# Kernel tuning notes

Measured on AMD Instinct MI355X. Metric: run time of the kernel, lower is better.

## Reference

```python
import jax, jax.numpy as jnp
import numpy as np


def _rx(state, theta, axis):
    # Apply RX(theta) to qubit at tensor axis `axis`. state: (B, 2,...,2) complex.
    half = theta * 0.5
    c = jnp.cos(half)
    s = jnp.sin(half)
    a0 = jnp.take(state, 0, axis=axis)
    a1 = jnp.take(state, 1, axis=axis)
    return jnp.stack([c * a0 - 1j * s * a1, c * a1 - 1j * s * a0], axis=axis)


def _cnot(state, w):
    # CNOT with control wire w (axis w+1), target wire w+1 (axis w+2).
    c_ax = w + 1
    s0 = jnp.take(state, 0, axis=c_ax)
    # after removing the control axis, the target axis index becomes c_ax
    s1 = jnp.flip(jnp.take(state, 1, axis=c_ax), axis=c_ax)
    return jnp.stack([s0, s1], axis=c_ax)


def _run_circuit(x, params):
    # x: (B, n) encoding angles; params: (depth, n) trainable RX angles.
    B, n = x.shape
    depth = params.shape[0]
    state = jnp.zeros((B,) + (2,) * n, jnp.complex64)
    state = state.at[(slice(None),) + (0,) * n].set(1.0 + 0.0j)
    # angle encoding: RX(x_w) on each wire
    for w in range(n):
        theta = x[:, w].reshape((B,) + (1,) * (n - 1))
        state = _rx(state, theta, w + 1)
    # variational layers: RX(param) per wire, then CNOT chain
    for d in range(depth):
        for w in range(n):
            state = _rx(state, params[d, w], w + 1)
        for w in range(n - 1):
            state = _cnot(state, w)
    probs = state.real ** 2 + state.imag ** 2  # (B, 2,...,2)
    ez = []
    for w in range(n):
        axes = tuple(a for a in range(1, n + 1) if a != w + 1)
        p = probs.sum(axes)  # (B, 2)
        ez.append(p[:, 0] - p[:, 1])  # <Z_w>
    return jnp.stack(ez, axis=1)  # (B, n)


def setup_inputs() -> dict:
    key = jax.random.key(0)
    k0, k1, k2, k3, k4 = jax.random.split(key, 5)
    seq_len, batch, input_dim = 256, 128, 64
    n_qubits, depth, hidden = 10, 2, 256
    inputs = jax.random.normal(k0, (seq_len, batch, input_dim), jnp.float32)
    mask = jax.random.randint(k1, (seq_len, batch), 0, 2).astype(jnp.int32)
    qparams = jax.random.normal(k2, (4, depth, n_qubits), jnp.float32)
    W = jax.random.normal(k3, (4, hidden, n_qubits), jnp.float32) / np.sqrt(n_qubits)
    b = jax.random.normal(k4, (4, hidden), jnp.float32) * 0.01
    return {"inputs": inputs, "mask": mask, "qparams": qparams, "W": W, "b": b}


def reference(inputs, mask, qparams, W, b):
    seq_len, batch, _ = inputs.shape
    n = qparams.shape[-1]
    hidden = W.shape[1]
    maskf = mask.astype(inputs.dtype)

    circuits4 = jax.vmap(_run_circuit, in_axes=(None, 0))  # over the 4 gates

    def step(carry, xm):
        hx, cx = carry
        x_t, m_t = xm
        q_in = jnp.concatenate([x_t, hx], axis=1)[:, :n]  # (B, n)
        z = circuits4(q_in, qparams)                      # (4, B, n)
        pre = jnp.einsum('gbn,ghn->gbh', z, W) + b[:, None, :]
        f = jax.nn.sigmoid(pre[0])
        i = jax.nn.sigmoid(pre[1])
        g = jnp.tanh(pre[2])
        o = jax.nn.sigmoid(pre[3])
        m = m_t[:, None]
        f = f * m + (1.0 - m)
        i = i * m
        g = g * m
        o = o * m + (1.0 - m)
        cx_new = f * cx + i * g
        hx_new = o * jnp.tanh(cx_new)
        return (hx_new, cx_new), hx_new

    h0 = jnp.zeros((batch, hidden), inputs.dtype)
    c0 = jnp.zeros((batch, hidden), inputs.dtype)
    (hx, cx), outputs = jax.lax.scan(jax.checkpoint(step), (h0, c0), (inputs, maskf))
    return outputs, (hx, cx)
```

## Files before the change

kernel.cpp:

```cpp
#include <hip/hip_runtime.h>

#define T_LEN 256
#define BATCH 128
#define NQ 10
#define HID 256
#define OUT_HX (T_LEN * BATCH * HID)
#define OUT_CX (OUT_HX + BATCH * HID)
#define TROW 33

#define KS  (-1.44269504089f)
#define KT2 (-2.88539008178f)

__global__ __launch_bounds__(256) void zker(
    const float* __restrict__ inputs,
    const float* __restrict__ qparams,
    float* __restrict__ zws)
{
  const int b   = blockIdx.x;
  const int tq  = blockIdx.y;
  const int tid = threadIdx.x;
  const int t   = tq * 64 + (tid >> 2);
  const int g   = tid & 3;

  const float sg = (g == 2) ? KT2 : KS;

  float th0[NQ], cth[NQ], sth[NQ];
#pragma unroll
  for (int k = 0; k < NQ; ++k) {
    th0[k]   = qparams[g * 2 * NQ + k];
    float t1 = qparams[g * 2 * NQ + NQ + k];
    sth[k] = __sinf(t1);
    cth[k] = __cosf(t1);
  }
  float cphi[NQ], sphi[NQ];
  const float* xp = inputs + (t * BATCH + b) * 64;
#pragma unroll
  for (int k = 0; k < NQ; ++k) {
    float ang = xp[k] + th0[k];
    sphi[k] = __sinf(ang);
    cphi[k] = __cosf(ang);
  }
  float* zout = zws + (b * NQ * T_LEN + t) * 4 + g;
#pragma unroll
  for (int w = 0; w < NQ; ++w) {
    float vI, vZ, vY, vX; int js;
    if (w == NQ - 1) { vI = 0.f; vZ = cth[NQ-1]; vY = sth[NQ-1]; vX = 0.f; js = NQ - 2; }
    else             { vI = 1.f; vZ = 0.f; vY = 0.f; vX = 0.f; js = w; }
#pragma unroll
    for (int j = js; j >= 0; --j) {
      float nI = cth[j] * (cphi[j+1] * vZ - sphi[j+1] * vY);
      float nZ = cth[j] * vI;
      float nY = sth[j] * vX;
      float nX = -sth[j] * (sphi[j+1] * vZ + cphi[j+1] * vY);
      vI = nI; vZ = nZ; vY = nY; vX = nX;
    }
    zout[w * T_LEN * 4] = (vI + cphi[0] * vZ - sphi[0] * vY) * sg;
  }
}

__global__ __launch_bounds__(512) void scanker(
    const float* __restrict__ zws,
    const int*  __restrict__ mask,
    const float* __restrict__ W,
    const float* __restrict__ bias,
    float* __restrict__ out)
{
  const int b    = blockIdx.x;
  const int h0   = blockIdx.y * 32;
  const int tid  = threadIdx.x;
  const int lane = tid & 63;
  const int wavu = __builtin_amdgcn_readfirstlane(tid >> 6);

  __shared__ float tlds[2][64 * TROW];
  __shared__ float mk[T_LEN];

  for (int t = tid; t < T_LEN; t += 512) mk[t] = (float)mask[t * BATCH + b];
  __syncthreads();

  int srcA[6]; bool pm[6];
#pragma unroll
  for (int k = 0; k < 6; ++k) {
    const int d = 1 << k;
    pm[k]   = (lane >= d);
    srcA[k] = ((lane >= d) ? (lane - d) : lane) << 2;
  }

  float bsc[4][4];
#pragma unroll
  for (int hh = 0; hh < 4; ++hh) {
    const int h = __builtin_amdgcn_readfirstlane(h0 + wavu * 4 + hh);
    bsc[hh][0] = bias[0 * HID + h] * KS;
    bsc[hh][1] = bias[1 * HID + h] * KS;
    bsc[hh][2] = bias[2 * HID + h] * KT2;
    bsc[hh][3] = bias[3 * HID + h] * KS;
  }

  float carry[4];
#pragma unroll
  for (int i = 0; i < 4; ++i) carry[i] = 0.f;

  const float4* zg = (const float4*)zws + b * NQ * T_LEN;

  for (int r = 0; r < 4; ++r) {
    const int p = r & 1;
    const int t = r * 64 + lane;
    const float m = mk[t];
    const float onem = 1.f - m;

    float acc[4][4];
#pragma unroll
    for (int hh = 0; hh < 4; ++hh) {
      acc[hh][0] = bsc[hh][0]; acc[hh][1] = bsc[hh][1];
      acc[hh][2] = bsc[hh][2]; acc[hh][3] = bsc[hh][3];
    }
#pragma unroll
    for (int n = 0; n < NQ; ++n) {
      const float4 z = zg[n * T_LEN + t];
#pragma unroll
      for (int hh = 0; hh < 4; ++hh) {
        const int wb = __builtin_amdgcn_readfirstlane((h0 + wavu * 4 + hh) * NQ + n);
        acc[hh][0] = fmaf(z.x, W[0 * HID * NQ + wb], acc[hh][0]);
        acc[hh][1] = fmaf(z.y, W[1 * HID * NQ + wb], acc[hh][1]);
        acc[hh][2] = fmaf(z.z, W[2 * HID * NQ + wb], acc[hh][2]);
        acc[hh][3] = fmaf(z.w, W[3 * HID * NQ + wb], acc[hh][3]);
      }
    }

    float a4[4], w4[4], om4[4];
#pragma unroll
    for (int hh = 0; hh < 4; ++hh) {
      const float uf = __builtin_amdgcn_rcpf(1.f + __builtin_amdgcn_exp2f(acc[hh][0]));
      const float ui = __builtin_amdgcn_rcpf(1.f + __builtin_amdgcn_exp2f(acc[hh][1]));
      const float ug = __builtin_amdgcn_rcpf(1.f + __builtin_amdgcn_exp2f(acc[hh][2]));
      const float uo = __builtin_amdgcn_rcpf(1.f + __builtin_amdgcn_exp2f(acc[hh][3]));
      a4[hh]  = fmaf(m, uf, onem);
      w4[hh]  = m * ui * fmaf(2.f, ug, -1.f);
      om4[hh] = fmaf(m, uo, onem);
    }

#pragma unroll
    for (int k = 0; k < 6; ++k) {
#pragma unroll
      for (int hh = 0; hh < 4; ++hh) {
        float au = __int_as_float(
            __builtin_amdgcn_ds_bpermute(srcA[k], __float_as_int(a4[hh])));
        float wu = __int_as_float(
            __builtin_amdgcn_ds_bpermute(srcA[k], __float_as_int(w4[hh])));
        au = pm[k] ? au : 1.f;
        wu = pm[k] ? wu : 0.f;
        w4[hh] = fmaf(a4[hh], wu, w4[hh]);
        a4[hh] = a4[hh] * au;
      }
    }

#pragma unroll
    for (int hh = 0; hh < 4; ++hh) {
      const float ct = fmaf(a4[hh], carry[hh], w4[hh]);
      carry[hh] = __shfl(ct, 63, 64);
      const float ec = __builtin_amdgcn_exp2f(ct * KT2);
      const float tc = fmaf(2.f, __builtin_amdgcn_rcpf(1.f + ec), -1.f);
      const float hv = om4[hh] * tc;
      tlds[p][lane * TROW + wavu * 4 + hh] = hv;
      if (r == 3 && lane == 63) {
        const int h = h0 + wavu * 4 + hh;
        out[OUT_HX + b * HID + h] = hv;
        out[OUT_CX + b * HID + h] = ct;
      }
    }

    __syncthreads();
    {
      const int tt = tid >> 3, c = tid & 7;
      float4 v;
      v.x = tlds[p][tt * TROW + 4 * c + 0];
      v.y = tlds[p][tt * TROW + 4 * c + 1];
      v.z = tlds[p][tt * TROW + 4 * c + 2];
      v.w = tlds[p][tt * TROW + 4 * c + 3];
      *(float4*)&out[(r * 64 + tt) * (BATCH * HID) + b * HID + h0 + 4 * c] = v;
    }
  }
}

extern "C" void kernel_launch(void* const* d_in, const int* in_sizes, int n_in,
                              void* d_out, int out_size, void* d_ws, size_t ws_size,
                              hipStream_t stream)
{
  int ii = 0, im = 1, iq = 2, iw = 3, ib = 4;
  for (int i = 0; i < n_in; ++i) {
    switch (in_sizes[i]) {
      case 2097152: ii = i; break;
      case 32768:   im = i; break;
      case 80:      iq = i; break;
      case 10240:   iw = i; break;
      case 1024:    ib = i; break;
      default: break;
    }
  }
  const float* inputs  = (const float*)d_in[ii];
  const int*   mask    = (const int*)d_in[im];
  const float* qparams = (const float*)d_in[iq];
  const float* W       = (const float*)d_in[iw];
  const float* bias    = (const float*)d_in[ib];
  float*       out     = (float*)d_out;
  float*       zws     = (float*)d_ws;

  zker<<<dim3(BATCH, 4), dim3(256), 0, stream>>>(inputs, qparams, zws);
  scanker<<<dim3(BATCH, 8), dim3(512), 0, stream>>>(zws, mask, W, bias, out);
}
```

Baseline: 106.7 us.

## Scan four timesteps per lane with a single wave-wide prefix pass

Each lane now owns four consecutive timesteps and composes their affine cell recurrences serially in registers. A single 64-lane Hillis-Steele scan then covers all 256 timesteps, replacing four sequential 64-step scan rounds that each carried state between rounds. The last scan stage skips the unneeded multiplier permute, and the per-round LDS transpose and barrier become one 32x256 transpose written out once at the end. The cost is higher register pressure, since per-timestep a/w/om values for four timesteps must stay live, plus a larger shared-memory footprint.

```diff
diff --git a/kernel.cpp b/kernel.cpp
--- a/kernel.cpp
+++ b/kernel.cpp
@@ -6,7 +6,7 @@
 #define HID 256
 #define OUT_HX (T_LEN * BATCH * HID)
 #define OUT_CX (OUT_HX + BATCH * HID)
-#define TROW 33
+#define TCOL 260
 
 #define KS  (-1.44269504089f)
 #define KT2 (-2.88539008178f)
@@ -57,6 +57,8 @@
     zout[w * T_LEN * 4] = (vI + cphi[0] * vZ - sphi[0] * vY) * sg;
   }
 }
+
+#define BP(SRC, V) __int_as_float(__builtin_amdgcn_ds_bpermute((SRC), __float_as_int(V)))
 
 __global__ __launch_bounds__(512) void scanker(
     const float* __restrict__ zws,
@@ -71,7 +73,7 @@
   const int lane = tid & 63;
   const int wavu = __builtin_amdgcn_readfirstlane(tid >> 6);
 
-  __shared__ float tlds[2][64 * TROW];
+  __shared__ float tlds[32][TCOL];
   __shared__ float mk[T_LEN];
 
   for (int t = tid; t < T_LEN; t += 512) mk[t] = (float)mask[t * BATCH + b];
@@ -84,6 +86,8 @@
     pm[k]   = (lane >= d);
     srcA[k] = ((lane >= d) ? (lane - d) : lane) << 2;
   }
+  const int srcE = ((lane >= 1) ? (lane - 1) : 0) << 2;
+  const bool pe  = (lane >= 1);
 
   float bsc[4][4];
 #pragma unroll
@@ -95,18 +99,12 @@
     bsc[hh][3] = bias[3 * HID + h] * KS;
   }
 
-  float carry[4];
-#pragma unroll
-  for (int i = 0; i < 4; ++i) carry[i] = 0.f;
-
   const float4* zg = (const float4*)zws + b * NQ * T_LEN;
 
-  for (int r = 0; r < 4; ++r) {
-    const int p = r & 1;
-    const int t = r * 64 + lane;
-    const float m = mk[t];
-    const float onem = 1.f - m;
-
+  float a[4][4], w[4][4], om[4][4];
+#pragma unroll
+  for (int tt = 0; tt < 4; ++tt) {
+    const int t = lane * 4 + tt;
     float acc[4][4];
 #pragma unroll
     for (int hh = 0; hh < 4; ++hh) {
@@ -125,59 +123,90 @@
         acc[hh][3] = fmaf(z.w, W[3 * HID * NQ + wb], acc[hh][3]);
       }
     }
-
-    float a4[4], w4[4], om4[4];
+    const float m = mk[t];
+    const float onem = 1.f - m;
 #pragma unroll
     for (int hh = 0; hh < 4; ++hh) {
       const float uf = __builtin_amdgcn_rcpf(1.f + __builtin_amdgcn_exp2f(acc[hh][0]));
       const float ui = __builtin_amdgcn_rcpf(1.f + __builtin_amdgcn_exp2f(acc[hh][1]));
       const float ug = __builtin_amdgcn_rcpf(1.f + __builtin_amdgcn_exp2f(acc[hh][2]));
       const float uo = __builtin_amdgcn_rcpf(1.f + __builtin_amdgcn_exp2f(acc[hh][3]));
-      a4[hh]  = fmaf(m, uf, onem);
-      w4[hh]  = m * ui * fmaf(2.f, ug, -1.f);
-      om4[hh] = fmaf(m, uo, onem);
-    }
-
-#pragma unroll
-    for (int k = 0; k < 6; ++k) {
-#pragma unroll
-      for (int hh = 0; hh < 4; ++hh) {
-        float au = __int_as_float(
-            __builtin_amdgcn_ds_bpermute(srcA[k], __float_as_int(a4[hh])));
-        float wu = __int_as_float(
-            __builtin_amdgcn_ds_bpermute(srcA[k], __float_as_int(w4[hh])));
+      a[tt][hh]  = fmaf(m, uf, onem);
+      w[tt][hh]  = m * ui * fmaf(2.f, ug, -1.f);
+      om[tt][hh] = fmaf(m, uo, onem);
+    }
+  }
+
+  float A[4], Wc[4];
+#pragma unroll
+  for (int hh = 0; hh < 4; ++hh) {
+    A[hh]  = a[0][hh];
+    Wc[hh] = w[0][hh];
+#pragma unroll
+    for (int tt = 1; tt < 4; ++tt) {
+      Wc[hh] = fmaf(a[tt][hh], Wc[hh], w[tt][hh]);
+      A[hh]  = a[tt][hh] * A[hh];
+    }
+  }
+
+#pragma unroll
+  for (int k = 0; k < 6; ++k) {
+#pragma unroll
+    for (int hh = 0; hh < 4; ++hh) {
+      float wu = BP(srcA[k], Wc[hh]);
+      wu = pm[k] ? wu : 0.f;
+      if (k < 5) {
+        float au = BP(srcA[k], A[hh]);
         au = pm[k] ? au : 1.f;
-        wu = pm[k] ? wu : 0.f;
-        w4[hh] = fmaf(a4[hh], wu, w4[hh]);
-        a4[hh] = a4[hh] * au;
+        Wc[hh] = fmaf(A[hh], wu, Wc[hh]);
+        A[hh]  = A[hh] * au;
+      } else {
+        Wc[hh] = fmaf(A[hh], wu, Wc[hh]);
       }
     }
-
-#pragma unroll
-    for (int hh = 0; hh < 4; ++hh) {
-      const float ct = fmaf(a4[hh], carry[hh], w4[hh]);
-      carry[hh] = __shfl(ct, 63, 64);
-      const float ec = __builtin_amdgcn_exp2f(ct * KT2);
+  }
+
+  float cpre[4];
+#pragma unroll
+  for (int hh = 0; hh < 4; ++hh) {
+    const float pw = BP(srcE, Wc[hh]);
+    cpre[hh] = pe ? pw : 0.f;
+  }
+
+#pragma unroll
+  for (int hh = 0; hh < 4; ++hh) {
+    float c = cpre[hh];
+    float4 hv4;
+    float hvs[4];
+#pragma unroll
+    for (int tt = 0; tt < 4; ++tt) {
+      c = fmaf(a[tt][hh], c, w[tt][hh]);
+      const float ec = __builtin_amdgcn_exp2f(c * KT2);
       const float tc = fmaf(2.f, __builtin_amdgcn_rcpf(1.f + ec), -1.f);
-      const float hv = om4[hh] * tc;
-      tlds[p][lane * TROW + wavu * 4 + hh] = hv;
-      if (r == 3 && lane == 63) {
-        const int h = h0 + wavu * 4 + hh;
-        out[OUT_HX + b * HID + h] = hv;
-        out[OUT_CX + b * HID + h] = ct;
-      }
-    }
-
-    __syncthreads();
-    {
-      const int tt = tid >> 3, c = tid & 7;
-      float4 v;
-      v.x = tlds[p][tt * TROW + 4 * c + 0];
-      v.y = tlds[p][tt * TROW + 4 * c + 1];
-      v.z = tlds[p][tt * TROW + 4 * c + 2];
-      v.w = tlds[p][tt * TROW + 4 * c + 3];
-      *(float4*)&out[(r * 64 + tt) * (BATCH * HID) + b * HID + h0 + 4 * c] = v;
-    }
+      hvs[tt] = om[tt][hh] * tc;
+    }
+    hv4.x = hvs[0]; hv4.y = hvs[1]; hv4.z = hvs[2]; hv4.w = hvs[3];
+    const int hcol = wavu * 4 + hh;
+    *(float4*)&tlds[hcol][lane * 4] = hv4;
+    if (lane == 63) {
+      out[OUT_HX + b * HID + h0 + hcol] = hvs[3];
+      out[OUT_CX + b * HID + h0 + hcol] = c;
+    }
+  }
+
+  __syncthreads();
+
+  {
+    const int t  = tid >> 1;
+    const int hf = (tid & 1) * 16;
+    float v[16];
+#pragma unroll
+    for (int i = 0; i < 16; ++i) v[i] = tlds[hf + i][t];
+    float4* op = (float4*)&out[t * (BATCH * HID) + b * HID + h0 + hf];
+    op[0] = make_float4(v[0],  v[1],  v[2],  v[3]);
+    op[1] = make_float4(v[4],  v[5],  v[6],  v[7]);
+    op[2] = make_float4(v[8],  v[9],  v[10], v[11]);
+    op[3] = make_float4(v[12], v[13], v[14], v[15]);
   }
 }
 
```

Result: slower. 132.2 us (+23.9%).
